# Optimization experiments

Hardware: AMD Instinct MI355X
Metric: run time of the kernel (lower is better)

The kernel has to match this reference:

```python
import jax, jax.numpy as jnp
import numpy as np

N = 10000      # nodes
E = 640000     # directed edges
D = 128        # feature width
C = 10         # classes
G = 64         # graphs in batch


def setup_inputs() -> dict:
    key = jax.random.key(0)
    ks = jax.random.split(key, 9)
    x = jax.random.normal(ks[0], (N, D), dtype=jnp.float32)
    edge_index = jax.random.randint(ks[1], (2, E), 0, N, dtype=jnp.int64)
    batch = jnp.sort(jax.random.randint(ks[2], (N,), 0, G, dtype=jnp.int64))
    scale = 1.0 / np.sqrt(D)
    W1 = jax.random.normal(ks[3], (D, D), dtype=jnp.float32) * scale
    W2 = jax.random.normal(ks[4], (D, D), dtype=jnp.float32) * scale
    W3 = jax.random.normal(ks[5], (D, D), dtype=jnp.float32) * scale
    W4 = jax.random.normal(ks[6], (D, D), dtype=jnp.float32) * scale
    fc_w = jax.random.normal(ks[7], (D, C), dtype=jnp.float32) * scale
    fc_b = jnp.zeros((C,), dtype=jnp.float32)
    return {"x": x, "edge_index": edge_index, "batch": batch,
            "W1": W1, "W2": W2, "W3": W3, "W4": W4,
            "fc_w": fc_w, "fc_b": fc_b}


def _gcn_conv(x, src, dst, deg_inv_sqrt, W):
    # GCNConv: h = x @ W; aggregate D^{-1/2}(A+I)D^{-1/2} h; then ReLU (activation).
    h = x @ W                                        # [N, D]
    norm = deg_inv_sqrt[src] * deg_inv_sqrt[dst]     # [E]
    msgs = h[src] * norm[:, None]                    # gather + scale
    agg = jax.ops.segment_sum(msgs, dst, num_segments=N)
    agg = agg + h * (deg_inv_sqrt * deg_inv_sqrt)[:, None]  # self-loop term
    return jax.nn.relu(agg)


def reference(x, edge_index, batch, W1, W2, W3, W4, fc_w, fc_b):
    src, dst = edge_index[0], edge_index[1]
    # degree counting self-loops (A + I normalization)
    deg = jax.ops.segment_sum(jnp.ones((E,), x.dtype), dst, num_segments=N) + 1.0
    deg_inv_sqrt = jax.lax.rsqrt(deg)
    for W in (W1, W2, W3, W4):
        x = _gcn_conv(x, src, dst, deg_inv_sqrt, W)
    xr = jax.ops.segment_sum(x, batch, num_segments=G)   # global_add_pool
    logits = x @ fc_w + fc_b
    return jax.nn.log_softmax(logits, axis=1), xr
```

## Files before the change

kernel.cpp:

```cpp
#include <hip/hip_runtime.h>
#include <math.h>

#define N_NODES 10000
#define N_EDGES 640000
#define DIM     128
#define NCLS    10
#define NGRAPH  64
#define NB      157
#define BCAP    4608
#define EPB     4000
#define NPB     8

typedef unsigned int uint32;
typedef unsigned short ushort16;

__device__ __forceinline__ ushort16 f32_to_bf16_rne(float f) {
    uint32 u = __float_as_uint(f);
    u = (u + 0x7fffu + ((u >> 16) & 1u)) >> 16;
    return (ushort16)u;
}

__device__ __forceinline__ float blo(uint32 x) { return __uint_as_float(x << 16); }
__device__ __forceinline__ float bhi(uint32 x) { return __uint_as_float(x & 0xffff0000u); }

__global__ __launch_bounds__(256) void binA_gemm1(const int* __restrict__ src,
                                                  const int* __restrict__ dst,
                                                  int* __restrict__ gcursor,
                                                  uint32* __restrict__ bins,
                                                  const float* __restrict__ X,
                                                  const float* __restrict__ W,
                                                  ushort16* __restrict__ Gh) {
    __shared__ uint32 pk[EPB];
    __shared__ int cntS[NB], offS[NB], curS[NB], gposS[NB];

    if (blockIdx.x < 625) {
        int c    = threadIdx.x & 127;
        int rg   = threadIdx.x >> 7;
        int row0 = blockIdx.x * 16 + rg * 8;
        const float* xb = X + row0 * DIM;
        float acc[8] = {0.f, 0.f, 0.f, 0.f, 0.f, 0.f, 0.f, 0.f};
        for (int k = 0; k < DIM; k += 4) {
            float w0 = W[(k + 0) * DIM + c];
            float w1 = W[(k + 1) * DIM + c];
            float w2 = W[(k + 2) * DIM + c];
            float w3 = W[(k + 3) * DIM + c];
#pragma unroll
            for (int r = 0; r < 8; r++) {
                float4 xv = *(const float4*)(xb + r * DIM + k);
                acc[r] += xv.x * w0 + xv.y * w1 + xv.z * w2 + xv.w * w3;
            }
        }
#pragma unroll
        for (int r = 0; r < 8; r++)
            Gh[(row0 + r) * DIM + c] = f32_to_bf16_rne(acc[r]);
        return;
    }

    int ab  = blockIdx.x - 625;
    int tid = threadIdx.x;
    for (int i = tid; i < NB; i += 256) cntS[i] = 0;
    __syncthreads();

    int base = ab * EPB;
    uint32 pr[16];
#pragma unroll
    for (int it = 0; it < 16; it++) {
        int i = it * 256 + tid;
        uint32 p = 0xffffffffu;
        if (i < EPB) {
            int e = base + i;
            p = ((uint32)dst[e] << 16) | (uint32)src[e];
            atomicAdd(&cntS[p >> 22], 1);
        }
        pr[it] = p;
    }
    __syncthreads();

    if (tid < 64) {
        int carry = 0;
        for (int r = 0; r < 3; r++) {
            int idx = r * 64 + tid;
            int v = (idx < NB) ? cntS[idx] : 0;
            int inc = v;
#pragma unroll
            for (int o = 1; o < 64; o <<= 1) {
                int u = __shfl_up(inc, o, 64);
                if (tid >= o) inc += u;
            }
            if (idx < NB) { offS[idx] = inc - v + carry; curS[idx] = inc - v + carry; }
            carry += __shfl(inc, 63, 64);
        }
    }
    __syncthreads();

#pragma unroll
    for (int it = 0; it < 16; it++) {
        uint32 p = pr[it];
        if (p != 0xffffffffu) {
            int b = p >> 22;
            pk[atomicAdd(&curS[b], 1)] = p;
        }
    }
    __syncthreads();

    if (tid < NB) gposS[tid] = atomicAdd(&gcursor[tid], cntS[tid]);
    __syncthreads();

#pragma unroll
    for (int it = 0; it < 16; it++) {
        int i = it * 256 + tid;
        if (i < EPB) {
            uint32 u = pk[i];
            int b = u >> 22;
            int gp = gposS[b] + (i - offS[b]);
            if (gp < BCAP) bins[b * BCAP + gp] = u;
        }
    }
}

__global__ __launch_bounds__(256) void binB(const int* __restrict__ gcursor,
                                            const uint32* __restrict__ bins,
                                            ushort16* __restrict__ col,
                                            int* __restrict__ deg,
                                            float* __restrict__ dis) {
    __shared__ ushort16 adj[64 * 128];
    __shared__ int cnt2[64];
    int b   = blockIdx.x;
    int tid = threadIdx.x;
    if (tid < 64) cnt2[tid] = 0;
    __syncthreads();
    int tc = gcursor[b];
    if (tc > BCAP) tc = BCAP;
    const uint32* bb = bins + b * BCAP;
    for (int i = tid; i < tc; i += 256) {
        uint32 u = bb[i];
        int local = (u >> 16) & 63;
        int r = atomicAdd(&cnt2[local], 1);
        if (r < 128) adj[(local << 7) + r] = (ushort16)(u & 0xffffu);
    }
    __syncthreads();
    uint4* dstp = (uint4*)(col + (size_t)b * 64 * 128);
    const uint4* srcp = (const uint4*)adj;
    for (int j = tid; j < 1024; j += 256) dstp[j] = srcp[j];
    if (tid < 64) {
        int node = b * 64 + tid;
        int c = cnt2[tid] < 128 ? cnt2[tid] : 128;
        deg[node] = c;
        dis[node] = rsqrtf((float)c + 1.0f);
    }
}

template <bool SCALED_IN>
__device__ __forceinline__ void agg_to_lds(const ushort16* __restrict__ Gh,
                                           const int* __restrict__ deg,
                                           const ushort16* __restrict__ col,
                                           const float* __restrict__ dis,
                                           float* __restrict__ Xs) {
    int tid  = threadIdx.x;
    int wave = tid >> 6;
    int lane = tid & 63;
    int grp  = lane >> 4;
    int sl   = lane & 15;
    const uint32* g32 = (const uint32*)Gh;
    const uint32* gp  = g32 + (sl << 2);

#pragma unroll
    for (int i = 0; i < 2; i++) {
        int vr = wave * 2 + i;
        int v  = blockIdx.x * NPB + vr;
        int dv = deg[v];
        uint32 colpack = ((const uint32*)(col + ((size_t)v << 7)))[lane];
        float acc[8];
#pragma unroll
        for (int j = 0; j < 8; j++) acc[j] = 0.f;

        int kk = 0;
        for (; kk + 8 <= dv; kk += 8) {
            int k0 = kk + grp, k1 = kk + 4 + grp;
            uint32 cp0 = __shfl(colpack, k0 >> 1, 64);
            uint32 cp1 = __shfl(colpack, k1 >> 1, 64);
            int u0 = (k0 & 1) ? (int)(cp0 >> 16) : (int)(cp0 & 0xffffu);
            int u1 = (k1 & 1) ? (int)(cp1 >> 16) : (int)(cp1 & 0xffffu);
            uint4 w0 = *(const uint4*)(gp + (u0 << 6));
            uint4 w1 = *(const uint4*)(gp + (u1 << 6));
            if (SCALED_IN) {
                acc[0] += blo(w0.x); acc[1] += bhi(w0.x);
                acc[2] += blo(w0.y); acc[3] += bhi(w0.y);
                acc[4] += blo(w0.z); acc[5] += bhi(w0.z);
                acc[6] += blo(w0.w); acc[7] += bhi(w0.w);
                acc[0] += blo(w1.x); acc[1] += bhi(w1.x);
                acc[2] += blo(w1.y); acc[3] += bhi(w1.y);
                acc[4] += blo(w1.z); acc[5] += bhi(w1.z);
                acc[6] += blo(w1.w); acc[7] += bhi(w1.w);
            } else {
                float s0 = dis[u0], s1 = dis[u1];
                acc[0] += s0 * blo(w0.x); acc[1] += s0 * bhi(w0.x);
                acc[2] += s0 * blo(w0.y); acc[3] += s0 * bhi(w0.y);
                acc[4] += s0 * blo(w0.z); acc[5] += s0 * bhi(w0.z);
                acc[6] += s0 * blo(w0.w); acc[7] += s0 * bhi(w0.w);
                acc[0] += s1 * blo(w1.x); acc[1] += s1 * bhi(w1.x);
                acc[2] += s1 * blo(w1.y); acc[3] += s1 * bhi(w1.y);
                acc[4] += s1 * blo(w1.z); acc[5] += s1 * bhi(w1.z);
                acc[6] += s1 * blo(w1.w); acc[7] += s1 * bhi(w1.w);
            }
        }
        for (; kk < dv; kk += 4) {
            int k = kk + grp;
            uint32 cp = __shfl(colpack, (k >> 1) & 63, 64);
            int u = (k & 1) ? (int)(cp >> 16) : (int)(cp & 0xffffu);
            if (k < dv) {
                uint4 w = *(const uint4*)(gp + (u << 6));
                float s = SCALED_IN ? 1.f : dis[u];
                acc[0] += s * blo(w.x); acc[1] += s * bhi(w.x);
                acc[2] += s * blo(w.y); acc[3] += s * bhi(w.y);
                acc[4] += s * blo(w.z); acc[5] += s * bhi(w.z);
                acc[6] += s * blo(w.w); acc[7] += s * bhi(w.w);
            }
        }
#pragma unroll
        for (int j = 0; j < 8; j++) {
            acc[j] += __shfl_xor(acc[j], 16, 64);
            acc[j] += __shfl_xor(acc[j], 32, 64);
        }
        float sv = dis[v];
        uint4 hs = *(const uint4*)(gp + (v << 6));
        float fs = SCALED_IN ? 1.f : sv;
        float r0 = sv * (acc[0] + fs * blo(hs.x));
        float r1 = sv * (acc[1] + fs * bhi(hs.x));
        float r2 = sv * (acc[2] + fs * blo(hs.y));
        float r3 = sv * (acc[3] + fs * bhi(hs.y));
        float r4 = sv * (acc[4] + fs * blo(hs.z));
        float r5 = sv * (acc[5] + fs * bhi(hs.z));
        float r6 = sv * (acc[6] + fs * blo(hs.w));
        float r7 = sv * (acc[7] + fs * bhi(hs.w));
        if (grp == 0) {
            float4* o = (float4*)(Xs + vr * DIM + sl * 8);
            o[0] = make_float4(fmaxf(r0, 0.f), fmaxf(r1, 0.f),
                               fmaxf(r2, 0.f), fmaxf(r3, 0.f));
            o[1] = make_float4(fmaxf(r4, 0.f), fmaxf(r5, 0.f),
                               fmaxf(r6, 0.f), fmaxf(r7, 0.f));
        }
    }
}

template <bool SCALED_IN>
__global__ __launch_bounds__(256) void fused_layer(const ushort16* __restrict__ Gh_in,
                                                   const int* __restrict__ deg,
                                                   const ushort16* __restrict__ col,
                                                   const float* __restrict__ dis,
                                                   const float* __restrict__ W,
                                                   ushort16* __restrict__ Gh_out) {
    __shared__ float Xs[NPB * DIM];
    agg_to_lds<SCALED_IN>(Gh_in, deg, col, dis, Xs);
    __syncthreads();

    int c  = threadIdx.x & 127;
    int rg = threadIdx.x >> 7;
    int row0 = blockIdx.x * NPB + rg * 4;
    float acc[4] = {0.f, 0.f, 0.f, 0.f};
    for (int k = 0; k < DIM; k += 4) {
        float w0 = W[(k + 0) * DIM + c];
        float w1 = W[(k + 1) * DIM + c];
        float w2 = W[(k + 2) * DIM + c];
        float w3 = W[(k + 3) * DIM + c];
#pragma unroll
        for (int r = 0; r < 4; r++) {
            float4 xv = *(const float4*)(Xs + (rg * 4 + r) * DIM + k);
            acc[r] += xv.x * w0 + xv.y * w1 + xv.z * w2 + xv.w * w3;
        }
    }
#pragma unroll
    for (int r = 0; r < 4; r++) {
        int row = row0 + r;
        Gh_out[row * DIM + c] = f32_to_bf16_rne(acc[r] * dis[row]);
    }
}

__global__ __launch_bounds__(256) void fused_last(const ushort16* __restrict__ Gh_in,
                                                  const int* __restrict__ deg,
                                                  const ushort16* __restrict__ col,
                                                  const float* __restrict__ dis,
                                                  const int* __restrict__ batch,
                                                  const float* __restrict__ fcw,
                                                  const float* __restrict__ fcb,
                                                  float* __restrict__ xr,
                                                  float* __restrict__ out) {
    __shared__ float Xs[NPB * DIM];
    agg_to_lds<true>(Gh_in, deg, col, dis, Xs);
    __syncthreads();

    int wave = threadIdx.x >> 6;
    int lane = threadIdx.x & 63;
#pragma unroll
    for (int i = 0; i < 2; i++) {
        int vr   = wave * 2 + i;
        int node = blockIdx.x * NPB + vr;
        float xl = Xs[vr * DIM + lane];
        float xh = Xs[vr * DIM + 64 + lane];
        float lg[NCLS];
#pragma unroll
        for (int c2 = 0; c2 < NCLS; c2++) {
            float p = xl * fcw[lane * NCLS + c2] + xh * fcw[(lane + 64) * NCLS + c2];
#pragma unroll
            for (int off = 32; off >= 1; off >>= 1) p += __shfl_xor(p, off, 64);
            lg[c2] = p + fcb[c2];
        }
        float m = lg[0];
#pragma unroll
        for (int c2 = 1; c2 < NCLS; c2++) m = fmaxf(m, lg[c2]);
        float s = 0.f;
#pragma unroll
        for (int c2 = 0; c2 < NCLS; c2++) s += expf(lg[c2] - m);
        float lse = m + logf(s);
        if (lane < NCLS) out[node * NCLS + lane] = lg[lane] - lse;
    }

    if (threadIdx.x < 128) {
        int start = blockIdx.x * NPB;
        int t = threadIdx.x;
        int b = batch[start];
        float a = 0.f;
        for (int n = 0; n < NPB; n++) {
            int bn = batch[start + n];
            if (bn != b) { atomicAdd(&xr[b * DIM + t], a); a = 0.f; b = bn; }
            a += Xs[n * DIM + t];
        }
        atomicAdd(&xr[b * DIM + t], a);
    }
}


extern "C" void kernel_launch(void* const* d_in, const int* in_sizes, int n_in,
                              void* d_out, int out_size, void* d_ws, size_t ws_size,
                              hipStream_t stream) {
    const float* x     = (const float*)d_in[0];
    const int*   ei    = (const int*)d_in[1];
    const int*   src   = ei;
    const int*   dst   = ei + N_EDGES;
    const int*   batch = (const int*)d_in[2];
    const float* W[4]  = {(const float*)d_in[3], (const float*)d_in[4],
                          (const float*)d_in[5], (const float*)d_in[6]};
    const float* fcw   = (const float*)d_in[7];
    const float* fcb   = (const float*)d_in[8];

    float* out_ls = (float*)d_out;
    float* out_xr = out_ls + N_NODES * NCLS;

    int*      gcursor = (int*)d_ws;
    int*      deg     = gcursor + 256;
    float*    dis     = (float*)(deg + 10240);
    uint32*   bins    = (uint32*)(dis + 10240);
    ushort16* col     = (ushort16*)(bins + NB * BCAP);
    ushort16* Gh_a    = col + (size_t)NB * 64 * 128;
    ushort16* Gh_b    = Gh_a + (size_t)N_NODES * DIM;

    hipMemsetAsync(gcursor, 0, 256 * sizeof(int), stream);
    hipMemsetAsync(out_xr, 0, NGRAPH * DIM * sizeof(float), stream);

    binA_gemm1<<<785, 256, 0, stream>>>(src, dst, gcursor, bins, x, W[0], Gh_a);
    binB      <<<NB, 256, 0, stream>>>(gcursor, bins, col, deg, dis);

    fused_layer<false><<<N_NODES / NPB, 256, 0, stream>>>(Gh_a, deg, col, dis, W[1], Gh_b);
    fused_layer<true> <<<N_NODES / NPB, 256, 0, stream>>>(Gh_b, deg, col, dis, W[2], Gh_a);
    fused_layer<true> <<<N_NODES / NPB, 256, 0, stream>>>(Gh_a, deg, col, dis, W[3], Gh_b);
    fused_last        <<<N_NODES / NPB, 256, 0, stream>>>(Gh_b, deg, col, dis, batch,
                                                          fcw, fcb, out_xr, out_ls);
}
```

Before: 198.3 us.

## Split-K fused layer GEMM, deeper gather unroll, fold xr memset into kernel

Three changes. The xr zeroing moves from a separate memset into an extra block of the first kernel, which removes one launch. The aggregation gather loop is unrolled to process 16 neighbours per step, so more independent row loads are in flight. The per-layer GEMM now splits K across the two thread groups, each covering all 8 rows, and combines the partial sums through LDS. That halves the W loads per thread but adds a second barrier, 4KB of extra shared memory and more registers.

```diff
diff --git a/kernel.cpp b/kernel.cpp
--- a/kernel.cpp
+++ b/kernel.cpp
@@ -29,7 +29,8 @@
                                                   uint32* __restrict__ bins,
                                                   const float* __restrict__ X,
                                                   const float* __restrict__ W,
-                                                  ushort16* __restrict__ Gh) {
+                                                  ushort16* __restrict__ Gh,
+                                                  float* __restrict__ xr) {
     __shared__ uint32 pk[EPB];
     __shared__ int cntS[NB], offS[NB], curS[NB], gposS[NB];
 
@@ -53,6 +54,13 @@
 #pragma unroll
         for (int r = 0; r < 8; r++)
             Gh[(row0 + r) * DIM + c] = f32_to_bf16_rne(acc[r]);
+        return;
+    }
+
+    if (blockIdx.x == 785) {
+        float4 z = make_float4(0.f, 0.f, 0.f, 0.f);
+        for (int j = threadIdx.x; j < NGRAPH * DIM / 4; j += 256)
+            ((float4*)xr)[j] = z;
         return;
     }
 
@@ -175,14 +183,20 @@
         for (int j = 0; j < 8; j++) acc[j] = 0.f;
 
         int kk = 0;
-        for (; kk + 8 <= dv; kk += 8) {
-            int k0 = kk + grp, k1 = kk + 4 + grp;
+        for (; kk + 16 <= dv; kk += 16) {
+            int k0 = kk + grp, k1 = kk + 4 + grp, k2 = kk + 8 + grp, k3 = kk + 12 + grp;
             uint32 cp0 = __shfl(colpack, k0 >> 1, 64);
             uint32 cp1 = __shfl(colpack, k1 >> 1, 64);
+            uint32 cp2 = __shfl(colpack, k2 >> 1, 64);
+            uint32 cp3 = __shfl(colpack, k3 >> 1, 64);
             int u0 = (k0 & 1) ? (int)(cp0 >> 16) : (int)(cp0 & 0xffffu);
             int u1 = (k1 & 1) ? (int)(cp1 >> 16) : (int)(cp1 & 0xffffu);
+            int u2 = (k2 & 1) ? (int)(cp2 >> 16) : (int)(cp2 & 0xffffu);
+            int u3 = (k3 & 1) ? (int)(cp3 >> 16) : (int)(cp3 & 0xffffu);
             uint4 w0 = *(const uint4*)(gp + (u0 << 6));
             uint4 w1 = *(const uint4*)(gp + (u1 << 6));
+            uint4 w2 = *(const uint4*)(gp + (u2 << 6));
+            uint4 w3 = *(const uint4*)(gp + (u3 << 6));
             if (SCALED_IN) {
                 acc[0] += blo(w0.x); acc[1] += bhi(w0.x);
                 acc[2] += blo(w0.y); acc[3] += bhi(w0.y);
@@ -192,8 +206,16 @@
                 acc[2] += blo(w1.y); acc[3] += bhi(w1.y);
                 acc[4] += blo(w1.z); acc[5] += bhi(w1.z);
                 acc[6] += blo(w1.w); acc[7] += bhi(w1.w);
+                acc[0] += blo(w2.x); acc[1] += bhi(w2.x);
+                acc[2] += blo(w2.y); acc[3] += bhi(w2.y);
+                acc[4] += blo(w2.z); acc[5] += bhi(w2.z);
+                acc[6] += blo(w2.w); acc[7] += bhi(w2.w);
+                acc[0] += blo(w3.x); acc[1] += bhi(w3.x);
+                acc[2] += blo(w3.y); acc[3] += bhi(w3.y);
+                acc[4] += blo(w3.z); acc[5] += bhi(w3.z);
+                acc[6] += blo(w3.w); acc[7] += bhi(w3.w);
             } else {
-                float s0 = dis[u0], s1 = dis[u1];
+                float s0 = dis[u0], s1 = dis[u1], s2 = dis[u2], s3 = dis[u3];
                 acc[0] += s0 * blo(w0.x); acc[1] += s0 * bhi(w0.x);
                 acc[2] += s0 * blo(w0.y); acc[3] += s0 * bhi(w0.y);
                 acc[4] += s0 * blo(w0.z); acc[5] += s0 * bhi(w0.z);
@@ -202,7 +224,34 @@
                 acc[2] += s1 * blo(w1.y); acc[3] += s1 * bhi(w1.y);
                 acc[4] += s1 * blo(w1.z); acc[5] += s1 * bhi(w1.z);
                 acc[6] += s1 * blo(w1.w); acc[7] += s1 * bhi(w1.w);
+                acc[0] += s2 * blo(w2.x); acc[1] += s2 * bhi(w2.x);
+                acc[2] += s2 * blo(w2.y); acc[3] += s2 * bhi(w2.y);
+                acc[4] += s2 * blo(w2.z); acc[5] += s2 * bhi(w2.z);
+                acc[6] += s2 * blo(w2.w); acc[7] += s2 * bhi(w2.w);
+                acc[0] += s3 * blo(w3.x); acc[1] += s3 * bhi(w3.x);
+                acc[2] += s3 * blo(w3.y); acc[3] += s3 * bhi(w3.y);
+                acc[4] += s3 * blo(w3.z); acc[5] += s3 * bhi(w3.z);
+                acc[6] += s3 * blo(w3.w); acc[7] += s3 * bhi(w3.w);
             }
+        }
+        for (; kk + 8 <= dv; kk += 8) {
+            int k0 = kk + grp, k1 = kk + 4 + grp;
+            uint32 cp0 = __shfl(colpack, k0 >> 1, 64);
+            uint32 cp1 = __shfl(colpack, k1 >> 1, 64);
+            int u0 = (k0 & 1) ? (int)(cp0 >> 16) : (int)(cp0 & 0xffffu);
+            int u1 = (k1 & 1) ? (int)(cp1 >> 16) : (int)(cp1 & 0xffffu);
+            uint4 w0 = *(const uint4*)(gp + (u0 << 6));
+            uint4 w1 = *(const uint4*)(gp + (u1 << 6));
+            float s0 = SCALED_IN ? 1.f : dis[u0];
+            float s1 = SCALED_IN ? 1.f : dis[u1];
+            acc[0] += s0 * blo(w0.x); acc[1] += s0 * bhi(w0.x);
+            acc[2] += s0 * blo(w0.y); acc[3] += s0 * bhi(w0.y);
+            acc[4] += s0 * blo(w0.z); acc[5] += s0 * bhi(w0.z);
+            acc[6] += s0 * blo(w0.w); acc[7] += s0 * bhi(w0.w);
+            acc[0] += s1 * blo(w1.x); acc[1] += s1 * bhi(w1.x);
+            acc[2] += s1 * blo(w1.y); acc[3] += s1 * bhi(w1.y);
+            acc[4] += s1 * blo(w1.z); acc[5] += s1 * bhi(w1.z);
+            acc[6] += s1 * blo(w1.w); acc[7] += s1 * bhi(w1.w);
         }
         for (; kk < dv; kk += 4) {
             int k = kk + grp;
@@ -251,28 +300,38 @@
                                                    const float* __restrict__ W,
                                                    ushort16* __restrict__ Gh_out) {
     __shared__ float Xs[NPB * DIM];
+    __shared__ float Cs[NPB * DIM];
     agg_to_lds<SCALED_IN>(Gh_in, deg, col, dis, Xs);
     __syncthreads();
 
     int c  = threadIdx.x & 127;
     int rg = threadIdx.x >> 7;
-    int row0 = blockIdx.x * NPB + rg * 4;
-    float acc[4] = {0.f, 0.f, 0.f, 0.f};
-    for (int k = 0; k < DIM; k += 4) {
-        float w0 = W[(k + 0) * DIM + c];
-        float w1 = W[(k + 1) * DIM + c];
-        float w2 = W[(k + 2) * DIM + c];
-        float w3 = W[(k + 3) * DIM + c];
-#pragma unroll
-        for (int r = 0; r < 4; r++) {
-            float4 xv = *(const float4*)(Xs + (rg * 4 + r) * DIM + k);
+    const float* Wh = W + rg * 64 * DIM;
+    const float* Xh = Xs + rg * 64;
+    float acc[8] = {0.f, 0.f, 0.f, 0.f, 0.f, 0.f, 0.f, 0.f};
+    for (int k = 0; k < 64; k += 4) {
+        float w0 = Wh[(k + 0) * DIM + c];
+        float w1 = Wh[(k + 1) * DIM + c];
+        float w2 = Wh[(k + 2) * DIM + c];
+        float w3 = Wh[(k + 3) * DIM + c];
+#pragma unroll
+        for (int r = 0; r < 8; r++) {
+            float4 xv = *(const float4*)(Xh + r * DIM + k);
             acc[r] += xv.x * w0 + xv.y * w1 + xv.z * w2 + xv.w * w3;
         }
     }
-#pragma unroll
-    for (int r = 0; r < 4; r++) {
-        int row = row0 + r;
-        Gh_out[row * DIM + c] = f32_to_bf16_rne(acc[r] * dis[row]);
+    if (rg == 1) {
+#pragma unroll
+        for (int r = 0; r < 8; r++) Cs[r * DIM + c] = acc[r];
+    }
+    __syncthreads();
+    if (rg == 0) {
+#pragma unroll
+        for (int r = 0; r < 8; r++) {
+            int row = blockIdx.x * NPB + r;
+            float s = acc[r] + Cs[r * DIM + c];
+            Gh_out[row * DIM + c] = f32_to_bf16_rne(s * dis[row]);
+        }
     }
 }
 
@@ -355,9 +414,8 @@
     ushort16* Gh_b    = Gh_a + (size_t)N_NODES * DIM;
 
     hipMemsetAsync(gcursor, 0, 256 * sizeof(int), stream);
-    hipMemsetAsync(out_xr, 0, NGRAPH * DIM * sizeof(float), stream);
-
-    binA_gemm1<<<785, 256, 0, stream>>>(src, dst, gcursor, bins, x, W[0], Gh_a);
+
+    binA_gemm1<<<786, 256, 0, stream>>>(src, dst, gcursor, bins, x, W[0], Gh_a, out_xr);
     binB      <<<NB, 256, 0, stream>>>(gcursor, bins, col, deg, dis);
 
     fused_layer<false><<<N_NODES / NPB, 256, 0, stream>>>(Gh_a, deg, col, dis, W[1], Gh_b);
```

Result: faster. 193.2 us (-2.6%).
